# Performance work log

Hardware: AMD Instinct MI355X
Metric: run time of the kernel (lower is better)

## Reference

```python
import jax, jax.numpy as jnp
import numpy as np

EPS = 1e-5  # F.layer_norm default eps
H_STEP = 0.1


def double_layer(x, K1, K2):
    # x: [1, Cin, N]; K1: [Cmid, Cin]; K2: [Cout, Cmid]  (1x1 conv1d == matmul)
    x = jnp.einsum('oc,bcn->bon', K1, x)
    # F.layer_norm(x, x.shape): normalize over the whole tensor, no affine
    m = jnp.mean(x)
    v = jnp.mean((x - m) ** 2)
    x = jnp.tanh((x - m) * jax.lax.rsqrt(v + EPS))
    return jnp.einsum('oc,bcn->bon', K2, x)


def setup_inputs() -> dict:
    key = jax.random.key(0)
    ks = jax.random.split(key, 12)
    N = 4096; nNin = 64; nopen = 256; nhid = 256; nNclose = 256
    nlayer = 8; num_output = 1024; E0 = 16 * N
    stdv = 1e-3
    return {
        'xn': jax.random.normal(ks[0], (1, nNin, N), jnp.float32),
        'K1Nopen': jax.random.normal(ks[1], (nopen, nNin), jnp.float32) * stdv,
        'K2Nopen': jax.random.normal(ks[2], (nopen, nopen), jnp.float32) * stdv,
        'KNclose': jax.random.normal(ks[3], (nNclose, nopen), jnp.float32) * stdv,
        'KN1': jax.random.uniform(ks[4], (nlayer, nhid, 2 * nopen), jnp.float32) * stdv,
        'KN2': jax.random.uniform(ks[5], (nlayer, nopen, nhid), jnp.float32) * stdv,
        'lin1_w': jax.random.normal(ks[6], (nopen, nopen), jnp.float32) / np.sqrt(nopen),
        'lin1_b': jnp.zeros((nopen,), jnp.float32),
        'lin2_w': jax.random.normal(ks[7], (num_output, nopen), jnp.float32) / np.sqrt(nopen),
        'lin2_b': jnp.zeros((num_output,), jnp.float32),
        'edge_i': jax.random.randint(ks[8], (E0,), 0, N),
        'edge_j': jax.random.randint(ks[9], (E0,), 0, N),
    }


def reference(xn, K1Nopen, K2Nopen, KNclose, KN1, KN2,
              lin1_w, lin1_b, lin2_w, lin2_b, edge_i, edge_j):
    N = xn.shape[-1]
    # gcn_norm's add_remaining_self_loops: input edge list has no self loops,
    # so append one per node once (fixed shapes; D[i,i] == exp(0) == 1 == fill).
    I = jnp.concatenate([edge_i, jnp.arange(N)])
    J = jnp.concatenate([edge_j, jnp.arange(N)])

    xn = double_layer(xn, K1Nopen, K2Nopen)  # [1, nopen, N]
    nlayers = KN1.shape[0]
    for i in range(nlayers):
        # --- updateGraph: dense pairwise Gaussian affinity, then gcn_norm ---
        f = xn[0]                          # [C, N]
        sq = jnp.sum(f * f, axis=0)        # [N]
        D = jax.nn.relu(sq[None, :] + sq[:, None] - 2.0 * (f.T @ f))  # [N, N]
        D = jnp.exp(-2.0 * (D / jnp.std(D, ddof=1)))
        w = D[I, J]                                          # gather edge affinities
        deg = jax.ops.segment_sum(w, J, num_segments=N)
        dis = jnp.where(deg > 0, jax.lax.rsqrt(deg), 0.0)
        W = dis[I] * w * dis[J]                              # normalized edge weights [E]
        # --- nodeLap = edgeDiv(nodeGrad(xn)) ---
        g = W[None, None, :] * (xn[:, :, I] - xn[:, :, J])   # nodeGrad [1, C, E]
        wg = (W[None, None, :] * g)[0].T                     # [E, C]
        lap = (jax.ops.segment_sum(wg, I, num_segments=N)
               - jax.ops.segment_sum(wg, J, num_segments=N)).T[None]  # [1, C, N]
        dxn = jnp.concatenate([xn, lap], axis=1)             # varlet features [1, 2C, N]
        dxn = double_layer(dxn, KN1[i], KN2[i])              # [1, C, N]
        xn = xn + H_STEP * dxn                               # heat update

    xn = jnp.einsum('oc,bcn->bon', KNclose, xn)[0].T         # [N, nNclose]
    x = jax.nn.elu(xn @ lin1_w.T + lin1_b)
    x = x @ lin2_w.T + lin2_b
    return jax.nn.log_softmax(x, axis=1)                     # [N, num_output]
```

## Files before the change

### kernel.cpp

```cpp
#include <hip/hip_runtime.h>
#include <hip/hip_bf16.h>

#define N_NODES 4096
#define CF      256
#define CIN     64
#define E0_EDGES 65536
#define NLAYER  8
#define NOUT    1024
#define CN      (CF * N_NODES)
#define STD_BLOCKS 64

typedef unsigned short ushort;
typedef __attribute__((ext_vector_type(8))) short s8v;
typedef __attribute__((ext_vector_type(4))) float f4v;

__device__ __forceinline__ ushort f2bf(float x){
  unsigned int u = __builtin_bit_cast(unsigned int, x);
  return (ushort)((u + 0x7FFFu + ((u >> 16) & 1u)) >> 16);
}
__device__ __forceinline__ float bf2f(ushort h){
  unsigned int u = ((unsigned int)h) << 16;
  return __builtin_bit_cast(float, u);
}

__device__ __forceinline__ float waveSumF(float v){
  #pragma unroll
  for (int o = 32; o; o >>= 1) v += __shfl_xor(v, o);
  return v;
}
__device__ __forceinline__ double waveSumD(double v){
  #pragma unroll
  for (int o = 32; o; o >>= 1) v += __shfl_xor(v, o);
  return v;
}
__device__ __forceinline__ float waveMaxF(float v){
  #pragma unroll
  for (int o = 32; o; o >>= 1) v = fmaxf(v, __shfl_xor(v, o));
  return v;
}
__device__ float blockSumF(float v){
  __shared__ float sm[4];
  v = waveSumF(v);
  int l = threadIdx.x & 63, w = threadIdx.x >> 6;
  __syncthreads();
  if (l == 0) sm[w] = v;
  __syncthreads();
  return sm[0] + sm[1] + sm[2] + sm[3];
}
__device__ double blockSumD(double v){
  __shared__ double sm[4];
  v = waveSumD(v);
  int l = threadIdx.x & 63, w = threadIdx.x >> 6;
  __syncthreads();
  if (l == 0) sm[w] = v;
  __syncthreads();
  return sm[0] + sm[1] + sm[2] + sm[3];
}
__device__ float blockMaxF(float v){
  __shared__ float sm[4];
  v = waveMaxF(v);
  int l = threadIdx.x & 63, w = threadIdx.x >> 6;
  __syncthreads();
  if (l == 0) sm[w] = v;
  __syncthreads();
  return fmaxf(fmaxf(sm[0], sm[1]), fmaxf(sm[2], sm[3]));
}

#define MF(a,b,c) c = __builtin_amdgcn_mfma_f32_16x16x32_bf16(a, b, c, 0, 0, 0)

template<int BK, int ACT, bool WF32, bool WBF, bool WFH, bool MV>
__global__ __launch_bounds__(256)
void gemmB1(const ushort* __restrict__ A1, const ushort* __restrict__ A2,
            int lda, int splitAt,
            const ushort* __restrict__ B, int ldb,
            float* __restrict__ Cf, ushort* __restrict__ Cb, ushort* __restrict__ Cfh,
            int ldc, size_t cStrideZ, int kChunk,
            float alpha, float beta, const float* __restrict__ bias,
            double* __restrict__ pS, double* __restrict__ pS2)
{
  constexpr int NC = BK / 32;
  __shared__ ushort As[2][64][BK + 8], Bs[2][64][BK + 8];
  const int tid = threadIdx.x;
  const int r  = tid >> 2;
  const int kq = (tid & 3) * (BK / 4);
  const int row0 = blockIdx.y * 64, col0 = blockIdx.x * 64;
  const int kStart = blockIdx.z * kChunk;
  const int nT = kChunk / BK;

  const int wid = tid >> 6, lane = tid & 63;
  const int wr = (wid >> 1) * 32, wc = (wid & 1) * 32;
  const int fr = lane & 15, fk = (lane >> 4) * 8;

  f4v acc[2][2] = {};
  s8v ra[NC], rb[NC];

#define LOADTILE(T) { \
    int k0 = kStart + (T) * BK; \
    const ushort* Ag; int kk; \
    if (k0 < splitAt) { Ag = A1; kk = k0; } else { Ag = A2; kk = k0 - splitAt; } \
    size_t aoff = (size_t)(row0 + r) * lda + kk + kq; \
    size_t boff = (size_t)(col0 + r) * ldb + k0 + kq; \
    _Pragma("unroll") \
    for (int c = 0; c < NC; c++) { \
      ra[c] = *(const s8v*)(A1 + 0, Ag + aoff + 8 * c); \
      rb[c] = *(const s8v*)(B + boff + 8 * c); } }

#define STORETILE(BUF) { \
    _Pragma("unroll") \
    for (int c = 0; c < NC; c++) { \
      *(s8v*)&As[BUF][r][kq + 8 * c] = ra[c]; \
      *(s8v*)&Bs[BUF][r][kq + 8 * c] = rb[c]; } }

  LOADTILE(0);
  STORETILE(0);

  for (int t = 0; t < nT; t++) {
    const int cur = t & 1;
    if (t + 1 < nT) LOADTILE(t + 1);
    __syncthreads();
    #pragma unroll
    for (int ks = 0; ks < BK; ks += 32) {
      s8v a0 = *(const s8v*)&As[cur][wr + fr][ks + fk];
      s8v a1 = *(const s8v*)&As[cur][wr + 16 + fr][ks + fk];
      s8v b0 = *(const s8v*)&Bs[cur][wc + fr][ks + fk];
      s8v b1 = *(const s8v*)&Bs[cur][wc + 16 + fr][ks + fk];
      MF(a0, b0, acc[0][0]);
      MF(a0, b1, acc[0][1]);
      MF(a1, b0, acc[1][0]);
      MF(a1, b1, acc[1][1]);
    }
    if (t + 1 < nT) STORETILE(cur ^ 1);
  }
#undef LOADTILE
#undef STORETILE

  double s = 0, s2 = 0;
  #pragma unroll
  for (int m = 0; m < 2; m++)
    #pragma unroll
    for (int n = 0; n < 2; n++) {
      const int rowb = row0 + wr + m * 16 + (lane >> 4) * 4;
      const int col  = col0 + wc + n * 16 + fr;
      ushort4 hv;
      #pragma unroll
      for (int q = 0; q < 4; q++) {
        size_t cidx = (size_t)(rowb + q) * ldc + col;
        float v = alpha * acc[m][n][q];
        if (cStrideZ) {
          Cf[blockIdx.z * cStrideZ + cidx] = v;
        } else {
          if (beta != 0.0f) v += beta * Cf[cidx];
          if (bias) v += bias[col];
          if (ACT == 1) v = (v > 0.0f) ? v : expm1f(v);
          if (WF32) Cf[cidx] = v;
          if (WBF)  Cb[cidx] = f2bf(v);
          if (WFH)  ((ushort*)&hv)[q] = f2bf(v);
          if (MV)   { s += v; s2 += (double)v * v; }
        }
      }
      if (WFH && !cStrideZ)
        *(ushort4*)(Cfh + (size_t)col * N_NODES + rowb) = hv;
    }
  if (MV) {
    s  = blockSumD(s);
    s2 = blockSumD(s2);
    if (tid == 0) {
      int bid = blockIdx.y * gridDim.x + blockIdx.x;
      pS[bid] = s; pS2[bid] = s2;
    }
  }
}

#define OFF_K1   0
#define OFF_K2   16384
#define OFF_KNC  81920
#define OFF_KN1  147456
#define OFF_KN2  1196032
#define OFF_L1   1720320
#define OFF_L2   1785856
#define NW_TOT   2048000

__global__ __launch_bounds__(256)
void prepWK(const float* s0, const float* s1, const float* s2, const float* s3,
            const float* s4, const float* s5, const float* s6,
            ushort* __restrict__ h)
{
  const int sizes[7] = {16384, 65536, 65536, 1048576, 524288, 65536, 262144};
  const int offs[7]  = {OFF_K1, OFF_K2, OFF_KNC, OFF_KN1, OFF_KN2, OFF_L1, OFF_L2};
  int seg = blockIdx.y;
  const float* src = seg==0?s0: seg==1?s1: seg==2?s2: seg==3?s3: seg==4?s4: seg==5?s5: s6;
  int n = sizes[seg], off = offs[seg];
  for (int i = blockIdx.x * 256 + threadIdx.x; i < n; i += gridDim.x * 256)
    h[off + i] = f2bf(src[i]);
}

__global__ __launch_bounds__(256)
void transposeBF(const float* __restrict__ in, ushort* __restrict__ outh, int R, int Cc)
{
  __shared__ float t[32][33];
  int x  = blockIdx.x * 32 + threadIdx.x;
  int y0 = blockIdx.y * 32;
  for (int dy = threadIdx.y; dy < 32; dy += 8)
    t[dy][threadIdx.x] = in[(size_t)(y0 + dy) * Cc + x];
  __syncthreads();
  int ox  = y0 + threadIdx.x;
  int oy0 = blockIdx.x * 32;
  for (int dy = threadIdx.y; dy < 32; dy += 8)
    outh[(size_t)(oy0 + dy) * R + ox] = f2bf(t[threadIdx.x][dy]);
}

__global__ __launch_bounds__(256)
void tanhNormBF(ushort* __restrict__ h, const double* __restrict__ pS,
                const double* __restrict__ pS2)
{
  __shared__ float bc[2];
  double a = pS[threadIdx.x], b = pS2[threadIdx.x];
  a = blockSumD(a);
  b = blockSumD(b);
  if (threadIdx.x == 0) {
    double m   = a / (double)CN;
    double var = b / (double)CN - m * m;
    bc[0] = (float)m;
    bc[1] = (float)(1.0 / sqrt(var + 1e-5));
  }
  __syncthreads();
  float mf = bc[0], rs = bc[1];
  for (size_t i = ((size_t)blockIdx.x * 256 + threadIdx.x) * 8; i < CN;
       i += (size_t)256 * 256 * 8) {
    s8v hv = *(s8v*)(h + i);
    #pragma unroll
    for (int k = 0; k < 8; k++) {
      float x = bf2f((ushort)hv[k]);
      x = tanhf((x - mf) * rs);
      hv[k] = (short)f2bf(x);
    }
    *(s8v*)(h + i) = hv;
  }
}

__global__ __launch_bounds__(256)
void sqSHK(const ushort* __restrict__ fTh, float* __restrict__ sq,
           float* __restrict__ sP, float* __restrict__ hP, float* __restrict__ deg)
{
  __shared__ float smS[4][256], smH[4][256];
  int b = blockIdx.x, w = threadIdx.x >> 6, lane = threadIdx.x & 63;
  if (threadIdx.x < 64) deg[b * 64 + threadIdx.x] = 0.0f;
  float sA[4] = {0,0,0,0}, hA[4] = {0,0,0,0};
  for (int rr = 0; rr < 16; rr++) {
    int n = b * 64 + rr * 4 + w;
    ushort4 u = ((const ushort4*)(fTh + (size_t)n * CF))[lane];
    float x0 = bf2f(u.x), x1 = bf2f(u.y), x2 = bf2f(u.z), x3 = bf2f(u.w);
    float q = waveSumF(x0*x0 + x1*x1 + x2*x2 + x3*x3);
    if (lane == 0) sq[n] = q;
    sA[0] += x0; sA[1] += x1; sA[2] += x2; sA[3] += x3;
    hA[0] += x0*q; hA[1] += x1*q; hA[2] += x2*q; hA[3] += x3*q;
  }
  #pragma unroll
  for (int k = 0; k < 4; k++) { smS[w][lane*4+k] = sA[k]; smH[w][lane*4+k] = hA[k]; }
  __syncthreads();
  int t = threadIdx.x;
  sP[(size_t)b * 256 + t] = smS[0][t] + smS[1][t] + smS[2][t] + smS[3][t];
  hP[(size_t)b * 256 + t] = smH[0][t] + smH[1][t] + smH[2][t] + smH[3][t];
}

__global__ __launch_bounds__(256)
void stdPartsK(const float* __restrict__ sP, const float* __restrict__ hP,
               const float* __restrict__ Gp, const float* __restrict__ sq,
               double* __restrict__ parts)
{
  int b = blockIdx.x, t = threadIdx.x;
  double S1 = 0, S2 = 0, sd = 0, hd = 0, gf = 0;
  for (int i = b * 256 + t; i < N_NODES; i += STD_BLOCKS * 256) {
    double q = sq[i]; S1 += q; S2 += q * q;
  }
  if (b == 0) {
    float sv = 0, hv = 0;
    for (int p = 0; p < 64; p++) { sv += sP[p * 256 + t]; hv += hP[p * 256 + t]; }
    sd = (double)sv * sv; hd = (double)hv * sv;
  }
  for (int i = b * 256 + t; i < CF * CF; i += STD_BLOCKS * 256) {
    double g = 0;
    #pragma unroll 4
    for (int z = 0; z < 16; z++) g += Gp[(size_t)z * 65536 + i];
    gf += g * g;
  }
  S1 = blockSumD(S1);
  S2 = blockSumD(S2);
  sd = blockSumD(sd);
  hd = blockSumD(hd);
  gf = blockSumD(gf);
  if (t == 0) {
    parts[0 * STD_BLOCKS + b] = S1;
    parts[1 * STD_BLOCKS + b] = S2;
    parts[2 * STD_BLOCKS + b] = sd;
    parts[3 * STD_BLOCKS + b] = hd;
    parts[4 * STD_BLOCKS + b] = gf;
  }
}

__global__ __launch_bounds__(256)
void edgeWK(const int* __restrict__ ei, const int* __restrict__ ej,
            const ushort* __restrict__ fTh, const float* __restrict__ sq,
            const double* __restrict__ parts, float* __restrict__ wE,
            float* __restrict__ deg)
{
  __shared__ float c0s;
  if (threadIdx.x < 64) {
    int l = threadIdx.x;
    double v0 = waveSumD(parts[0 * STD_BLOCKS + l]);
    double v1 = waveSumD(parts[1 * STD_BLOCKS + l]);
    double v2 = waveSumD(parts[2 * STD_BLOCKS + l]);
    double v3 = waveSumD(parts[3 * STD_BLOCKS + l]);
    double v4 = waveSumD(parts[4 * STD_BLOCKS + l]);
    if (l == 0) {
      double NN = (double)N_NODES;
      double sum1 = 2.0 * NN * v0 - 2.0 * v2;
      double sum2 = 2.0 * NN * v1 + 2.0 * v0 * v0 + 4.0 * v4 - 8.0 * v3;
      double n2 = NN * NN;
      double var = (sum2 - sum1 * sum1 / n2) / (n2 - 1.0);
      double sdev = sqrt(var > 0 ? var : 0);
      c0s = (float)(-2.0 / sdev);
    }
  }
  __syncthreads();
  float c0 = c0s;
  int w = threadIdx.x >> 6, lane = threadIdx.x & 63;
  int e0 = (blockIdx.x * 4 + w) * 4;
  for (int q = 0; q < 4; q++) {
    int e = e0 + q;
    int i = ei[e], j = ej[e];
    ushort4 ua = ((const ushort4*)(fTh + (size_t)i * CF))[lane];
    ushort4 ub = ((const ushort4*)(fTh + (size_t)j * CF))[lane];
    float d = waveSumF(bf2f(ua.x)*bf2f(ub.x) + bf2f(ua.y)*bf2f(ub.y) +
                       bf2f(ua.z)*bf2f(ub.z) + bf2f(ua.w)*bf2f(ub.w));
    if (lane == 0) {
      float dist = fmaxf(sq[i] + sq[j] - 2.0f * d, 0.0f);
      float ww = expf(c0 * dist);
      wE[e] = ww;
      unsafeAtomicAdd(&deg[j], ww);
    }
  }
}

__global__ __launch_bounds__(256)
void csrCountK(const int* __restrict__ ei, const int* __restrict__ ej,
               int* __restrict__ cntO, int* __restrict__ cntI)
{
  int e = blockIdx.x * 256 + threadIdx.x;
  atomicAdd(&cntO[ei[e]], 1);
  atomicAdd(&cntI[ej[e]], 1);
}

__global__ __launch_bounds__(256)
void csrScanK(const int* __restrict__ cntO, const int* __restrict__ cntI,
              int* __restrict__ ofsO, int* __restrict__ ofsI)
{
  __shared__ int smO[256], smI[256];
  int t = threadIdx.x;
  int lo[16], li[16];
  int sO = 0, sI = 0;
  #pragma unroll
  for (int k = 0; k < 16; k++) {
    lo[k] = cntO[t * 16 + k]; li[k] = cntI[t * 16 + k];
    sO += lo[k]; sI += li[k];
  }
  smO[t] = sO; smI[t] = sI;
  __syncthreads();
  for (int off = 1; off < 256; off <<= 1) {
    int aO = (t >= off) ? smO[t - off] : 0;
    int aI = (t >= off) ? smI[t - off] : 0;
    __syncthreads();
    smO[t] += aO; smI[t] += aI;
    __syncthreads();
  }
  int bO = smO[t] - sO;
  int bI = smI[t] - sI;
  #pragma unroll
  for (int k = 0; k < 16; k++) {
    ofsO[t * 16 + k] = bO; bO += lo[k];
    ofsI[t * 16 + k] = bI; bI += li[k];
  }
}

__global__ __launch_bounds__(256)
void csrFillK(const int* __restrict__ ei, const int* __restrict__ ej,
              const int* __restrict__ ofsO, const int* __restrict__ ofsI,
              int* __restrict__ curO, int* __restrict__ curI,
              int2* __restrict__ lstO, int2* __restrict__ lstI)
{
  int e = blockIdx.x * 256 + threadIdx.x;
  int i = ei[e], j = ej[e];
  int p = atomicAdd(&curO[i], 1); lstO[ofsO[i] + p] = make_int2(j, e);
  int q = atomicAdd(&curI[j], 1); lstI[ofsI[j] + q] = make_int2(i, e);
}

__global__ __launch_bounds__(256)
void gatherLapK(const int2* __restrict__ lstO, const int2* __restrict__ lstI,
                const int* __restrict__ ofsO, const int* __restrict__ ofsI,
                const int* __restrict__ cntO, const int* __restrict__ cntI,
                const float* __restrict__ wE, const float* __restrict__ deg,
                const ushort* __restrict__ fTh, ushort* __restrict__ lapTh)
{
  int n = blockIdx.x, c = threadIdx.x;
  float own = bf2f(fTh[(size_t)n * CF + c]);
  float dn = rsqrtf(1.0f + deg[n]);
  float acc = 0.0f;
  int o0 = ofsO[n], oc = cntO[n];
  for (int k = 0; k < oc; k++) {
    int2 oe = lstO[o0 + k];
    float W = dn * wE[oe.y] * rsqrtf(1.0f + deg[oe.x]);
    acc += (W * W) * (own - bf2f(fTh[(size_t)oe.x * CF + c]));
  }
  int i0 = ofsI[n], ic = cntI[n];
  for (int k = 0; k < ic; k++) {
    int2 oe = lstI[i0 + k];
    float W = rsqrtf(1.0f + deg[oe.x]) * wE[oe.y] * dn;
    acc -= (W * W) * (bf2f(fTh[(size_t)oe.x * CF + c]) - own);
  }
  lapTh[(size_t)n * CF + c] = f2bf(acc);
}

__global__ __launch_bounds__(256)
void logSoftmaxK(const float* __restrict__ logits, float* __restrict__ out)
{
  int n = blockIdx.x;
  const float* row = logits + (size_t)n * NOUT;
  float mx = -1e30f;
  for (int o = threadIdx.x; o < NOUT; o += 256) mx = fmaxf(mx, row[o]);
  mx = blockMaxF(mx);
  float se = 0;
  for (int o = threadIdx.x; o < NOUT; o += 256) se += expf(row[o] - mx);
  se = blockSumF(se);
  float lse = mx + logf(se);
  for (int o = threadIdx.x; o < NOUT; o += 256) out[(size_t)n * NOUT + o] = row[o] - lse;
}

extern "C" void kernel_launch(void* const* d_in, const int* in_sizes, int n_in,
                              void* d_out, int out_size, void* d_ws, size_t ws_size,
                              hipStream_t stream)
{
  (void)in_sizes; (void)n_in; (void)out_size; (void)ws_size;
  const float* x0      = (const float*)d_in[0];
  const float* K1      = (const float*)d_in[1];
  const float* K2      = (const float*)d_in[2];
  const float* KNclose = (const float*)d_in[3];
  const float* KN1     = (const float*)d_in[4];
  const float* KN2     = (const float*)d_in[5];
  const float* lin1w   = (const float*)d_in[6];
  const float* lin1b   = (const float*)d_in[7];
  const float* lin2w   = (const float*)d_in[8];
  const float* lin2b   = (const float*)d_in[9];
  const int*   ei      = (const int*)d_in[10];
  const int*   ej      = (const int*)d_in[11];
  float* out = (float*)d_out;

  float* base   = (float*)d_ws;
  float* fT     = base;
  float* logits = fT + (size_t)CN;
  float* Gp     = logits + 4 * (size_t)CN;
  float* sq     = Gp + (size_t)CN;
  float* deg    = sq + N_NODES;
  float* sP     = deg + N_NODES;
  float* hP     = sP + 64 * 256;
  float* wE     = hP + 64 * 256;
  double* pS    = (double*)(wE + E0_EDGES + 2);
  double* pS2   = pS + 256;
  double* parts = pS2 + 256;

  ushort* u0 = (ushort*)(((uintptr_t)(parts + 5 * STD_BLOCKS) + 15) & ~(uintptr_t)15);
  ushort* fTh   = u0;
  ushort* fh    = fTh + (size_t)CN;
  ushort* lapTh = fh + (size_t)CN;
  ushort* uTh   = lapTh + (size_t)CN;
  ushort* wH    = uTh + (size_t)CN;
  int* ib = (int*)(((uintptr_t)(wH + NW_TOT) + 15) & ~(uintptr_t)15);
  int*  cntO = ib;
  int*  cntI = cntO + N_NODES;
  int*  ofsO = cntI + N_NODES;
  int*  ofsI = ofsO + N_NODES;
  int*  curO = ofsI + N_NODES;
  int*  curI = curO + N_NODES;
  int2* lstO = (int2*)(curI + N_NODES);
  int2* lstI = lstO + E0_EDGES;

  prepWK<<<dim3(64, 7), 256, 0, stream>>>(K1, K2, KNclose, KN1, KN2, lin1w, lin2w, wH);
  hipMemsetAsync(cntO, 0, 6 * N_NODES * sizeof(int), stream);
  csrCountK<<<E0_EDGES/256, 256, 0, stream>>>(ei, ej, cntO, cntI);
  csrScanK<<<1, 256, 0, stream>>>(cntO, cntI, ofsO, ofsI);
  csrFillK<<<E0_EDGES/256, 256, 0, stream>>>(ei, ej, ofsO, ofsI, curO, curI, lstO, lstI);

  transposeBF<<<dim3(N_NODES/32, CIN/32), dim3(32, 8), 0, stream>>>(x0, fh, CIN, N_NODES);
  gemmB1<64,0,0,1,0,1><<<dim3(4,64,1), 256, 0, stream>>>(
      fh, fh, CIN, 1 << 30, wH + OFF_K1, CIN,
      nullptr, uTh, nullptr, CF, 0, CIN, 1.f, 0.f, nullptr, pS, pS2);
  tanhNormBF<<<256, 256, 0, stream>>>(uTh, pS, pS2);
  gemmB1<128,0,1,1,1,0><<<dim3(4,64,1), 256, 0, stream>>>(
      uTh, uTh, CF, 1 << 30, wH + OFF_K2, CF,
      fT, fTh, fh, CF, 0, CF, 1.f, 0.f, nullptr, nullptr, nullptr);

  for (int L = 0; L < NLAYER; L++) {
    const ushort* k1h = wH + OFF_KN1 + (size_t)L * CF * 2 * CF;
    const ushort* k2h = wH + OFF_KN2 + (size_t)L * CF * CF;

    sqSHK<<<64, 256, 0, stream>>>(fTh, sq, sP, hP, deg);
    gemmB1<128,0,1,0,0,0><<<dim3(4,4,16), 256, 0, stream>>>(
        fh, fh, N_NODES, 1 << 30, fh, N_NODES,
        Gp, nullptr, nullptr, CF, 65536, 256, 1.f, 0.f, nullptr, nullptr, nullptr);
    stdPartsK<<<STD_BLOCKS, 256, 0, stream>>>(sP, hP, Gp, sq, parts);
    edgeWK<<<E0_EDGES/16, 256, 0, stream>>>(ei, ej, fTh, sq, parts, wE, deg);
    gatherLapK<<<N_NODES, 256, 0, stream>>>(lstO, lstI, ofsO, ofsI, cntO, cntI,
                                            wE, deg, fTh, lapTh);
    gemmB1<128,0,0,1,0,1><<<dim3(4,64,1), 256, 0, stream>>>(
        fTh, lapTh, CF, 256, k1h, 2*CF,
        nullptr, uTh, nullptr, CF, 0, 2*CF, 1.f, 0.f, nullptr, pS, pS2);
    tanhNormBF<<<256, 256, 0, stream>>>(uTh, pS, pS2);
    gemmB1<128,0,1,1,1,0><<<dim3(4,64,1), 256, 0, stream>>>(
        uTh, uTh, CF, 1 << 30, k2h, CF,
        fT, fTh, fh, CF, 0, CF, 0.1f, 1.f, nullptr, nullptr, nullptr);
  }

  gemmB1<128,0,0,1,0,0><<<dim3(4,64,1), 256, 0, stream>>>(
      fTh, fTh, CF, 1 << 30, wH + OFF_KNC, CF,
      nullptr, uTh, nullptr, CF, 0, CF, 1.f, 0.f, nullptr, nullptr, nullptr);
  gemmB1<128,1,0,1,0,0><<<dim3(4,64,1), 256, 0, stream>>>(
      uTh, uTh, CF, 1 << 30, wH + OFF_L1, CF,
      nullptr, lapTh, nullptr, CF, 0, CF, 1.f, 0.f, lin1b, nullptr, nullptr);
  gemmB1<128,0,1,0,0,0><<<dim3(16,64,1), 256, 0, stream>>>(
      lapTh, lapTh, CF, 1 << 30, wH + OFF_L2, CF,
      logits, nullptr, nullptr, NOUT, 0, CF, 1.f, 0.f, lin2b, nullptr, nullptr);
  logSoftmaxK<<<N_NODES, 256, 0, stream>>>(logits, out);
}
```

Before: 885.1 us.

## Exploit Gram symmetry, precompute squared edge weights, vectorize Laplacian gather

The per-layer Gram matrix GEMM now computes only the 10 upper-triangular 64x64 tiles, and the std reduction weights off-diagonal entries by two. A new per-edge kernel precomputes squared normalized weights, so the Laplacian gather reads one value per edge. The gather itself now assigns one wavefront per node with ushort4 loads instead of one scalar thread per channel. The GEMM main loop is restructured into a two-tile register double buffer. Lower-triangle Gp entries are no longer written, which is fine only as long as nothing else reads them.

```diff
diff --git a/kernel.cpp b/kernel.cpp
--- a/kernel.cpp
+++ b/kernel.cpp
@@ -68,7 +68,7 @@
 
 #define MF(a,b,c) c = __builtin_amdgcn_mfma_f32_16x16x32_bf16(a, b, c, 0, 0, 0)
 
-template<int BK, int ACT, bool WF32, bool WBF, bool WFH, bool MV>
+template<int BK, int ACT, bool WF32, bool WBF, bool WFH, bool MV, bool TRI>
 __global__ __launch_bounds__(256)
 void gemmB1(const ushort* __restrict__ A1, const ushort* __restrict__ A2,
             int lda, int splitAt,
@@ -83,7 +83,13 @@
   const int tid = threadIdx.x;
   const int r  = tid >> 2;
   const int kq = (tid & 3) * (BK / 4);
-  const int row0 = blockIdx.y * 64, col0 = blockIdx.x * 64;
+  int bx = blockIdx.x, by = blockIdx.y;
+  if (TRI) {
+    const int trT[10] = {0,0,0,0,1,1,1,2,2,3};
+    const int tcT[10] = {0,1,2,3,1,2,3,2,3,3};
+    by = trT[blockIdx.x]; bx = tcT[blockIdx.x];
+  }
+  const int row0 = by * 64, col0 = bx * 64;
   const int kStart = blockIdx.z * kChunk;
   const int nT = kChunk / BK;
 
@@ -92,9 +98,9 @@
   const int fr = lane & 15, fk = (lane >> 4) * 8;
 
   f4v acc[2][2] = {};
-  s8v ra[NC], rb[NC];
-
-#define LOADTILE(T) { \
+  s8v rA0[NC], rB0[NC], rA1[NC], rB1[NC];
+
+#define LOADTILE(T, RA, RB) { \
     int k0 = kStart + (T) * BK; \
     const ushort* Ag; int kk; \
     if (k0 < splitAt) { Ag = A1; kk = k0; } else { Ag = A2; kk = k0 - splitAt; } \
@@ -102,37 +108,46 @@
     size_t boff = (size_t)(col0 + r) * ldb + k0 + kq; \
     _Pragma("unroll") \
     for (int c = 0; c < NC; c++) { \
-      ra[c] = *(const s8v*)(A1 + 0, Ag + aoff + 8 * c); \
-      rb[c] = *(const s8v*)(B + boff + 8 * c); } }
-
-#define STORETILE(BUF) { \
+      RA[c] = *(const s8v*)(Ag + aoff + 8 * c); \
+      RB[c] = *(const s8v*)(B + boff + 8 * c); } }
+
+#define STORETILE(BUF, RA, RB) { \
     _Pragma("unroll") \
     for (int c = 0; c < NC; c++) { \
-      *(s8v*)&As[BUF][r][kq + 8 * c] = ra[c]; \
-      *(s8v*)&Bs[BUF][r][kq + 8 * c] = rb[c]; } }
-
-  LOADTILE(0);
-  STORETILE(0);
-
-  for (int t = 0; t < nT; t++) {
-    const int cur = t & 1;
-    if (t + 1 < nT) LOADTILE(t + 1);
+      *(s8v*)&As[BUF][r][kq + 8 * c] = RA[c]; \
+      *(s8v*)&Bs[BUF][r][kq + 8 * c] = RB[c]; } }
+
+#define MFMAT(BUF) { \
+    _Pragma("unroll") \
+    for (int ks = 0; ks < BK; ks += 32) { \
+      s8v a0 = *(const s8v*)&As[BUF][wr + fr][ks + fk]; \
+      s8v a1 = *(const s8v*)&As[BUF][wr + 16 + fr][ks + fk]; \
+      s8v b0 = *(const s8v*)&Bs[BUF][wc + fr][ks + fk]; \
+      s8v b1 = *(const s8v*)&Bs[BUF][wc + 16 + fr][ks + fk]; \
+      MF(a0, b0, acc[0][0]); \
+      MF(a0, b1, acc[0][1]); \
+      MF(a1, b0, acc[1][0]); \
+      MF(a1, b1, acc[1][1]); } }
+
+  LOADTILE(0, rA0, rB0);
+  if (nT > 1) LOADTILE(1, rA1, rB1);
+  STORETILE(0, rA0, rB0);
+
+  for (int t = 0; t < nT; t += 2) {
     __syncthreads();
-    #pragma unroll
-    for (int ks = 0; ks < BK; ks += 32) {
-      s8v a0 = *(const s8v*)&As[cur][wr + fr][ks + fk];
-      s8v a1 = *(const s8v*)&As[cur][wr + 16 + fr][ks + fk];
-      s8v b0 = *(const s8v*)&Bs[cur][wc + fr][ks + fk];
-      s8v b1 = *(const s8v*)&Bs[cur][wc + 16 + fr][ks + fk];
-      MF(a0, b0, acc[0][0]);
-      MF(a0, b1, acc[0][1]);
-      MF(a1, b0, acc[1][0]);
-      MF(a1, b1, acc[1][1]);
+    if (t + 2 < nT) LOADTILE(t + 2, rA0, rB0);
+    MFMAT(0);
+    if (t + 1 < nT) {
+      STORETILE(1, rA1, rB1);
+      __syncthreads();
+      if (t + 3 < nT) LOADTILE(t + 3, rA1, rB1);
+      MFMAT(1);
+      if (t + 2 < nT) STORETILE(0, rA0, rB0);
     }
-    if (t + 1 < nT) STORETILE(cur ^ 1);
   }
 #undef LOADTILE
 #undef STORETILE
+#undef MFMAT
 
   double s = 0, s2 = 0;
   #pragma unroll
@@ -279,10 +294,12 @@
     sd = (double)sv * sv; hd = (double)hv * sv;
   }
   for (int i = b * 256 + t; i < CF * CF; i += STD_BLOCKS * 256) {
+    int r = i >> 8, c = i & 255;
+    if (r > c) continue;
     double g = 0;
     #pragma unroll 4
     for (int z = 0; z < 16; z++) g += Gp[(size_t)z * 65536 + i];
-    gf += g * g;
+    gf += (r == c) ? g * g : 2.0 * g * g;
   }
   S1 = blockSumD(S1);
   S2 = blockSumD(S2);
@@ -343,6 +360,16 @@
 }
 
 __global__ __launch_bounds__(256)
+void wsqK(const int* __restrict__ ei, const int* __restrict__ ej,
+          const float* __restrict__ wE, const float* __restrict__ deg,
+          float* __restrict__ Wsq)
+{
+  int e = blockIdx.x * 256 + threadIdx.x;
+  float W = rsqrtf(1.0f + deg[ei[e]]) * wE[e] * rsqrtf(1.0f + deg[ej[e]]);
+  Wsq[e] = W * W;
+}
+
+__global__ __launch_bounds__(256)
 void csrCountK(const int* __restrict__ ei, const int* __restrict__ ej,
                int* __restrict__ cntO, int* __restrict__ cntI)
 {
@@ -398,26 +425,33 @@
 void gatherLapK(const int2* __restrict__ lstO, const int2* __restrict__ lstI,
                 const int* __restrict__ ofsO, const int* __restrict__ ofsI,
                 const int* __restrict__ cntO, const int* __restrict__ cntI,
-                const float* __restrict__ wE, const float* __restrict__ deg,
+                const float* __restrict__ Wsq,
                 const ushort* __restrict__ fTh, ushort* __restrict__ lapTh)
 {
-  int n = blockIdx.x, c = threadIdx.x;
-  float own = bf2f(fTh[(size_t)n * CF + c]);
-  float dn = rsqrtf(1.0f + deg[n]);
-  float acc = 0.0f;
-  int o0 = ofsO[n], oc = cntO[n];
-  for (int k = 0; k < oc; k++) {
-    int2 oe = lstO[o0 + k];
-    float W = dn * wE[oe.y] * rsqrtf(1.0f + deg[oe.x]);
-    acc += (W * W) * (own - bf2f(fTh[(size_t)oe.x * CF + c]));
-  }
-  int i0 = ofsI[n], ic = cntI[n];
-  for (int k = 0; k < ic; k++) {
-    int2 oe = lstI[i0 + k];
-    float W = rsqrtf(1.0f + deg[oe.x]) * wE[oe.y] * dn;
-    acc -= (W * W) * (bf2f(fTh[(size_t)oe.x * CF + c]) - own);
-  }
-  lapTh[(size_t)n * CF + c] = f2bf(acc);
+  int w = threadIdx.x >> 6, lane = threadIdx.x & 63;
+  int n = blockIdx.x * 4 + w;
+  ushort4 u = ((const ushort4*)(fTh + (size_t)n * CF))[lane];
+  float o0 = bf2f(u.x), o1 = bf2f(u.y), o2 = bf2f(u.z), o3 = bf2f(u.w);
+  float a0 = 0, a1 = 0, a2 = 0, a3 = 0;
+  int p0 = ofsO[n], pc = cntO[n];
+  for (int k = 0; k < pc; k++) {
+    int2 oe = lstO[p0 + k];
+    float W2 = Wsq[oe.y];
+    ushort4 v = ((const ushort4*)(fTh + (size_t)oe.x * CF))[lane];
+    a0 += W2 * (o0 - bf2f(v.x)); a1 += W2 * (o1 - bf2f(v.y));
+    a2 += W2 * (o2 - bf2f(v.z)); a3 += W2 * (o3 - bf2f(v.w));
+  }
+  int q0 = ofsI[n], qc = cntI[n];
+  for (int k = 0; k < qc; k++) {
+    int2 oe = lstI[q0 + k];
+    float W2 = Wsq[oe.y];
+    ushort4 v = ((const ushort4*)(fTh + (size_t)oe.x * CF))[lane];
+    a0 += W2 * (o0 - bf2f(v.x)); a1 += W2 * (o1 - bf2f(v.y));
+    a2 += W2 * (o2 - bf2f(v.z)); a3 += W2 * (o3 - bf2f(v.w));
+  }
+  ushort4 rv;
+  rv.x = f2bf(a0); rv.y = f2bf(a1); rv.z = f2bf(a2); rv.w = f2bf(a3);
+  ((ushort4*)(lapTh + (size_t)n * CF))[lane] = rv;
 }
 
 __global__ __launch_bounds__(256)
@@ -463,7 +497,8 @@
   float* sP     = deg + N_NODES;
   float* hP     = sP + 64 * 256;
   float* wE     = hP + 64 * 256;
-  double* pS    = (double*)(wE + E0_EDGES + 2);
+  float* Wsq    = wE + E0_EDGES;
+  double* pS    = (double*)(Wsq + E0_EDGES + 2);
   double* pS2   = pS + 256;
   double* parts = pS2 + 256;
 
@@ -490,11 +525,11 @@
   csrFillK<<<E0_EDGES/256, 256, 0, stream>>>(ei, ej, ofsO, ofsI, curO, curI, lstO, lstI);
 
   transposeBF<<<dim3(N_NODES/32, CIN/32), dim3(32, 8), 0, stream>>>(x0, fh, CIN, N_NODES);
-  gemmB1<64,0,0,1,0,1><<<dim3(4,64,1), 256, 0, stream>>>(
+  gemmB1<64,0,0,1,0,1,false><<<dim3(4,64,1), 256, 0, stream>>>(
       fh, fh, CIN, 1 << 30, wH + OFF_K1, CIN,
       nullptr, uTh, nullptr, CF, 0, CIN, 1.f, 0.f, nullptr, pS, pS2);
   tanhNormBF<<<256, 256, 0, stream>>>(uTh, pS, pS2);
-  gemmB1<128,0,1,1,1,0><<<dim3(4,64,1), 256, 0, stream>>>(
+  gemmB1<128,0,1,1,1,0,false><<<dim3(4,64,1), 256, 0, stream>>>(
       uTh, uTh, CF, 1 << 30, wH + OFF_K2, CF,
       fT, fTh, fh, CF, 0, CF, 1.f, 0.f, nullptr, nullptr, nullptr);
 
@@ -503,29 +538,30 @@
     const ushort* k2h = wH + OFF_KN2 + (size_t)L * CF * CF;
 
     sqSHK<<<64, 256, 0, stream>>>(fTh, sq, sP, hP, deg);
-    gemmB1<128,0,1,0,0,0><<<dim3(4,4,16), 256, 0, stream>>>(
+    gemmB1<128,0,1,0,0,0,true><<<dim3(10,1,16), 256, 0, stream>>>(
         fh, fh, N_NODES, 1 << 30, fh, N_NODES,
         Gp, nullptr, nullptr, CF, 65536, 256, 1.f, 0.f, nullptr, nullptr, nullptr);
     stdPartsK<<<STD_BLOCKS, 256, 0, stream>>>(sP, hP, Gp, sq, parts);
     edgeWK<<<E0_EDGES/16, 256, 0, stream>>>(ei, ej, fTh, sq, parts, wE, deg);
-    gatherLapK<<<N_NODES, 256, 0, stream>>>(lstO, lstI, ofsO, ofsI, cntO, cntI,
-                                            wE, deg, fTh, lapTh);
-    gemmB1<128,0,0,1,0,1><<<dim3(4,64,1), 256, 0, stream>>>(
+    wsqK<<<E0_EDGES/256, 256, 0, stream>>>(ei, ej, wE, deg, Wsq);
+    gatherLapK<<<N_NODES/4, 256, 0, stream>>>(lstO, lstI, ofsO, ofsI, cntO, cntI,
+                                              Wsq, fTh, lapTh);
+    gemmB1<128,0,0,1,0,1,false><<<dim3(4,64,1), 256, 0, stream>>>(
         fTh, lapTh, CF, 256, k1h, 2*CF,
         nullptr, uTh, nullptr, CF, 0, 2*CF, 1.f, 0.f, nullptr, pS, pS2);
     tanhNormBF<<<256, 256, 0, stream>>>(uTh, pS, pS2);
-    gemmB1<128,0,1,1,1,0><<<dim3(4,64,1), 256, 0, stream>>>(
+    gemmB1<128,0,1,1,1,0,false><<<dim3(4,64,1), 256, 0, stream>>>(
         uTh, uTh, CF, 1 << 30, k2h, CF,
         fT, fTh, fh, CF, 0, CF, 0.1f, 1.f, nullptr, nullptr, nullptr);
   }
 
-  gemmB1<128,0,0,1,0,0><<<dim3(4,64,1), 256, 0, stream>>>(
+  gemmB1<128,0,0,1,0,0,false><<<dim3(4,64,1), 256, 0, stream>>>(
       fTh, fTh, CF, 1 << 30, wH + OFF_KNC, CF,
       nullptr, uTh, nullptr, CF, 0, CF, 1.f, 0.f, nullptr, nullptr, nullptr);
-  gemmB1<128,1,0,1,0,0><<<dim3(4,64,1), 256, 0, stream>>>(
+  gemmB1<128,1,0,1,0,0,false><<<dim3(4,64,1), 256, 0, stream>>>(
       uTh, uTh, CF, 1 << 30, wH + OFF_L1, CF,
       nullptr, lapTh, nullptr, CF, 0, CF, 1.f, 0.f, lin1b, nullptr, nullptr);
-  gemmB1<128,0,1,0,0,0><<<dim3(16,64,1), 256, 0, stream>>>(
+  gemmB1<128,0,1,0,0,0,false><<<dim3(16,64,1), 256, 0, stream>>>(
       lapTh, lapTh, CF, 1 << 30, wH + OFF_L2, CF,
       logits, nullptr, nullptr, NOUT, 0, CF, 1.f, 0.f, lin2b, nullptr, nullptr);
   logSoftmaxK<<<N_NODES, 256, 0, stream>>>(logits, out);
```

Result: faster. 820.7 us (-7.3%).
